# Optimization experiments

Hardware: AMD Instinct MI355X
Metric: run time of the kernel (lower is better)

Reference implementation:

```python
import jax, jax.numpy as jnp
import numpy as np

N, E, R, H = 50000, 400000, 3, 3
IN, HID, OUT, C, B = 128, 64, 64, 16, 8


def _deg_norm(idx):
    # DGL GraphConv norm='both': deg.clamp(min=1) ** -0.5
    deg = jax.ops.segment_sum(jnp.ones(idx.shape, jnp.float32), idx, N)
    return jnp.maximum(deg, 1.0) ** -0.5


def _graph_conv(h, W, b, s, d):
    # h: [N, ..., F_in]; norm by src out-degree, matmul, scatter-sum to dst, norm by dst in-degree
    ns, nd = _deg_norm(s), _deg_norm(d)
    bshape = (N,) + (1,) * (h.ndim - 1)
    hw = (h * ns.reshape(bshape)) @ W
    agg = jax.ops.segment_sum(hw[s], d, N)
    return agg * nd.reshape(bshape) + b


def _gat(h, W, al, ar, b, s, d):
    # h: [N, HID] -> [N, H, HID] multi-head GAT with edge softmax over incoming edges
    f = (h @ W).reshape(N, H, HID)
    el = jnp.sum(f * al, axis=-1)  # [N, H]
    er = jnp.sum(f * ar, axis=-1)  # [N, H]
    e = jax.nn.leaky_relu(el[s] + er[d], 0.2)  # [E, H]
    m = jax.ops.segment_max(e, d, N)
    ez = jnp.exp(e - m[d])
    z = jax.ops.segment_sum(ez, d, N)
    alpha = ez / (z[d] + 1e-9)  # [E, H]
    out = jax.ops.segment_sum(alpha[:, :, None] * f[s], d, N)  # [N, H, HID]
    return out + b.reshape(H, HID)


def setup_inputs() -> dict:
    key = jax.random.key(0)
    k = jax.random.split(key, 12)
    s = 0.05
    return {
        "x": jax.random.normal(k[0], (N, IN), jnp.float32),
        "src": jax.random.randint(k[1], (R, E), 0, N, jnp.int32),
        "dst": jax.random.randint(k[2], (R, E), 0, N, jnp.int32),
        "graph_id": (jnp.arange(N, dtype=jnp.int32) * B // N).astype(jnp.int32),
        "W1": jax.random.normal(k[3], (R, IN, HID), jnp.float32) * s,
        "b1": jnp.zeros((R, HID), jnp.float32),
        "Wg": jax.random.normal(k[4], (R, HID, H * HID), jnp.float32) * s,
        "al": jax.random.normal(k[5], (R, H, HID), jnp.float32) * s,
        "ar": jax.random.normal(k[6], (R, H, HID), jnp.float32) * s,
        "bg": jnp.zeros((R, H * HID), jnp.float32),
        "W2": jax.random.normal(k[7], (R, HID, OUT), jnp.float32) * s,
        "b2": jnp.zeros((R, OUT), jnp.float32),
        "Wc": jax.random.normal(k[8], (OUT, C), jnp.float32) * s,
        "bc": jnp.zeros((C,), jnp.float32),
    }


def reference(x, src, dst, graph_id, W1, b1, Wg, al, ar, bg, W2, b2, Wc, bc):
    # conv1: per-relation GraphConv, aggregate='sum'
    h = sum(_graph_conv(x, W1[r], b1[r], src[r], dst[r]) for r in range(R))  # [N, HID]
    # F.normalize (L2 over dim=1, eps=1e-12)
    h = h / jnp.maximum(jnp.linalg.norm(h, axis=1, keepdims=True), 1e-12)
    # gatconv: per-relation GAT (3 heads), aggregate='sum'
    h = sum(_gat(h, Wg[r], al[r], ar[r], bg[r], src[r], dst[r]) for r in range(R))  # [N, H, HID]
    h = jax.nn.relu(h)
    # dropout(0.3) omitted: deterministic eval reference
    # conv2: GraphConv applied per head
    h = sum(_graph_conv(h, W2[r], b2[r], src[r], dst[r]) for r in range(R))  # [N, H, OUT]
    h = jax.nn.sigmoid(h)
    # dgl.mean_nodes over batched graphs
    cnt = jax.ops.segment_sum(jnp.ones((N,), jnp.float32), graph_id, B)
    pooled = jax.ops.segment_sum(h, graph_id, B) / jnp.maximum(cnt, 1.0)[:, None, None]  # [B, H, OUT]
    hg = jax.nn.sigmoid(pooled @ Wc + bc)  # [B, H, C]
    return jnp.mean(hg, axis=2)  # [B, H]
```

## Files before the change

kernel.cpp:

```cpp
#include <hip/hip_runtime.h>
#include <math.h>

#define NN 50000
#define EE 400000
#define RR 3
#define NH 3
#define FIN 128
#define HID 64
#define FOUT 64
#define NC 16
#define NB 8
#define NGAT 208

typedef __attribute__((ext_vector_type(8))) short v8s;
typedef __attribute__((ext_vector_type(4))) float v4f;
typedef unsigned short u16;
typedef unsigned char u8;
typedef unsigned int u32;
typedef __attribute__((ext_vector_type(4))) unsigned short u16x4;

#define QS 32.0f
#define IQS (1.0f / 32.0f)

__device__ __forceinline__ u16 f2b(float f) {
  unsigned u = __float_as_uint(f);
  return (u16)((u + 0x7fffu + ((u >> 16) & 1u)) >> 16);
}
__device__ __forceinline__ float b2f(u16 b) {
  return __uint_as_float(((unsigned)b) << 16);
}
__device__ __forceinline__ float wexp(float e) {
  e = e > 0.f ? e : 0.2f * e;
  return __expf(e);
}
__device__ __forceinline__ u8 f2e(float v) {
  return (u8)(__builtin_amdgcn_cvt_pk_fp8_f32(v, 0.f, 0, false) & 0xff);
}

__global__ void k_deg(const int* __restrict__ src, const int* __restrict__ dst,
                      int* __restrict__ degs, int* __restrict__ degd) {
  int i = blockIdx.x * 256 + threadIdx.x;
  if (i >= RR * EE) return;
  int r = i / EE;
  atomicAdd(&degs[r * NN + src[i]], 1);
  atomicAdd(&degd[r * NN + dst[i]], 1);
}

__global__ void k_norm(const int* __restrict__ degs, const int* __restrict__ degd,
                       float* __restrict__ ns, float* __restrict__ nd) {
  int i = blockIdx.x * 256 + threadIdx.x;
  if (i >= RR * NN) return;
  ns[i] = 1.0f / sqrtf((float)(degs[i] > 1 ? degs[i] : 1));
  nd[i] = 1.0f / sqrtf((float)(degd[i] > 1 ? degd[i] : 1));
}

__global__ void k_scan1(const int* __restrict__ deg, int* __restrict__ offs,
                        int* __restrict__ bsum) {
  __shared__ int sh[256];
  int gid = blockIdx.x * 256 + threadIdx.x;
  int v = (gid < RR * NN) ? deg[gid] : 0;
  sh[threadIdx.x] = v;
  __syncthreads();
  for (int off = 1; off < 256; off <<= 1) {
    int t = (threadIdx.x >= off) ? sh[threadIdx.x - off] : 0;
    __syncthreads();
    sh[threadIdx.x] += t;
    __syncthreads();
  }
  if (gid < RR * NN) offs[gid] = sh[threadIdx.x] - v;
  if (threadIdx.x == 255) bsum[blockIdx.x] = sh[255];
}

__global__ void k_scan2(int* __restrict__ bsum, int nb) {
  __shared__ int sh[1024];
  int v = (threadIdx.x < nb) ? bsum[threadIdx.x] : 0;
  sh[threadIdx.x] = v;
  __syncthreads();
  for (int off = 1; off < 1024; off <<= 1) {
    int t = (threadIdx.x >= off) ? sh[threadIdx.x - off] : 0;
    __syncthreads();
    sh[threadIdx.x] += t;
    __syncthreads();
  }
  if (threadIdx.x < nb) bsum[threadIdx.x] = sh[threadIdx.x] - v;
}

__global__ void k_scan3(int* __restrict__ offs, const int* __restrict__ bsum,
                        int* __restrict__ cursor) {
  int i = blockIdx.x * 256 + threadIdx.x;
  if (i >= RR * NN) return;
  int v = offs[i] + bsum[i / 256];
  offs[i] = v;
  cursor[i] = v;
}

__global__ void k_fill(const int* __restrict__ src, const int* __restrict__ dst,
                       int* __restrict__ cursor, int* __restrict__ esrc,
                       int* __restrict__ edst) {
  int i = blockIdx.x * 256 + threadIdx.x;
  if (i >= RR * EE) return;
  int r = i / EE;
  int d = dst[i];
  int pos = atomicAdd(&cursor[r * NN + d], 1);
  esrc[pos] = src[i];
  edst[pos] = d;
}

__global__ void k_cast(const float4* __restrict__ in, u16x4* __restrict__ out, int n4) {
  int i = blockIdx.x * 256 + threadIdx.x;
  if (i >= n4) return;
  float4 v = in[i];
  u16x4 o;
  o.x = f2b(v.x); o.y = f2b(v.y); o.z = f2b(v.z); o.w = f2b(v.w);
  out[i] = o;
}

__global__ void k_bcomp(const float* __restrict__ Wg, const float* __restrict__ al,
                        const float* __restrict__ ar, float* __restrict__ B) {
  int i = blockIdx.x * 256 + threadIdx.x;
  if (i >= RR * HID * NGAT) return;
  int col = i % NGAT;
  int k = (i / NGAT) % HID;
  int r = i / (NGAT * HID);
  float v = 0.f;
  if (col < NH * HID) {
    v = Wg[((size_t)(r * HID + k)) * (NH * HID) + col];
  } else if (col < NH * HID + 6) {
    int c2 = col - NH * HID;
    int isar = c2 / NH, h = c2 % NH;
    const float* wg = Wg + ((size_t)(r * HID + k)) * (NH * HID) + h * HID;
    const float* av = (isar ? ar : al) + (r * NH + h) * HID;
    float a = 0.f;
#pragma unroll 8
    for (int c = 0; c < HID; ++c) a += wg[c] * av[c];
    v = a;
  }
  B[i] = v;
}

template <int K, int N, int OUTMODE>
__global__ __launch_bounds__(256) void k_gemm(const u16* __restrict__ A, int lda,
                                              const float* __restrict__ B0, int bstr,
                                              void* __restrict__ C0,
                                              u16* __restrict__ elr,
                                              const float* __restrict__ s0, int M) {
  constexpr int KP = K + 8;
  __shared__ __align__(16) u16 Bt[N * KP];
  int y = blockIdx.y;
  int rrel = (OUTMODE == 3) ? y / NH : y;
  int head = (OUTMODE == 3) ? y % NH : 0;
  const float* B = B0 + (size_t)rrel * bstr;
  const float* scale = s0 + (size_t)rrel * NN;
  const u16* Ab = A + head * HID;
  for (int i = threadIdx.x; i < K * N; i += 256) {
    int k = i / N, n = i % N;
    Bt[n * KP + k] = f2b(B[(size_t)k * N + n]);
  }
  __syncthreads();
  int wid = threadIdx.x >> 6, lane = threadIdx.x & 63;
  int l15 = lane & 15, lg = lane >> 4;
  constexpr int NT = N / 16;
  int ntiles = (M + 63) >> 6;
  for (int tile = blockIdx.x; tile < ntiles; tile += gridDim.x) {
    int mbase = tile * 64 + wid * 16;
    v4f acc[NT];
#pragma unroll
    for (int t = 0; t < NT; ++t) acc[t] = (v4f)(0.f);
    int arow = mbase + l15;
    if (arow >= M) arow = M - 1;
    const u16* ap = Ab + (size_t)arow * lda + lg * 8;
#pragma unroll
    for (int ks = 0; ks < K / 32; ++ks) {
      v8s a = *(const v8s*)(ap + ks * 32);
#pragma unroll
      for (int t = 0; t < NT; ++t) {
        v8s b = *(const v8s*)(&Bt[(t * 16 + l15) * KP + lg * 8 + ks * 32]);
        acc[t] = __builtin_amdgcn_mfma_f32_16x16x32_bf16(a, b, acc[t], 0, 0, 0);
      }
    }
#pragma unroll
    for (int q = 0; q < 4; ++q) {
      int row = mbase + lg * 4 + q;
      if (row >= M) continue;
      if (OUTMODE == 1) {
        float s = scale[row] * QS;
        u8* C = (u8*)C0 + ((size_t)y * M + row) * 64;
#pragma unroll
        for (int t = 0; t < NT; ++t) C[t * 16 + l15] = f2e(acc[t][q] * s);
      } else if (OUTMODE == 2) {
        u32* C = (u32*)C0 + ((size_t)y * M + row) * 64;
#pragma unroll
        for (int tm = 0; tm < 4; ++tm) {
          u32 pk = __builtin_amdgcn_cvt_pk_fp8_f32(acc[tm][q] * QS,
                                                   acc[tm + 4][q] * QS, 0, false);
          pk = __builtin_amdgcn_cvt_pk_fp8_f32(acc[tm + 8][q] * QS, 0.f, pk, true);
          C[tm * 16 + l15] = pk;
        }
        if (l15 < 6)
          elr[((size_t)y * M + row) * 8 + (l15 < 3 ? l15 : l15 + 1)] =
              f2b(acc[12][q]);
      } else {
        float s = scale[row] * QS;
        u8* C = (u8*)C0 + (((size_t)rrel * M + row) * 64) * 4 + head;
#pragma unroll
        for (int t = 0; t < NT; ++t) C[(t * 16 + l15) * 4] = f2e(acc[t][q] * s);
      }
    }
  }
}

__global__ void k_g1(const int* __restrict__ offs, const int* __restrict__ degd,
                     const int* __restrict__ esrc, const u8* __restrict__ c1pk,
                     const float* __restrict__ nd, const float* __restrict__ b1,
                     u16* __restrict__ h1b) {
  int node = blockIdx.x * 4 + (threadIdx.x >> 6);
  int lane = threadIdx.x & 63;
  if (node >= NN) return;
  float v = 0.f;
#pragma unroll
  for (int r = 0; r < RR; ++r) {
    int start = offs[r * NN + node];
    int deg = degd[r * NN + node];
    const u8* base = c1pk + (size_t)r * NN * 64 + lane;
    float t = 0.f;
    int j = 0;
    for (; j + 4 <= deg; j += 4) {
      int s0 = esrc[start + j], s1 = esrc[start + j + 1];
      int s2 = esrc[start + j + 2], s3 = esrc[start + j + 3];
      float a0 = __builtin_amdgcn_cvt_f32_fp8((u32)base[(size_t)s0 * 64], 0);
      float a1 = __builtin_amdgcn_cvt_f32_fp8((u32)base[(size_t)s1 * 64], 0);
      float a2 = __builtin_amdgcn_cvt_f32_fp8((u32)base[(size_t)s2 * 64], 0);
      float a3 = __builtin_amdgcn_cvt_f32_fp8((u32)base[(size_t)s3 * 64], 0);
      t += (a0 + a1) + (a2 + a3);
    }
    for (; j < deg; ++j)
      t += __builtin_amdgcn_cvt_f32_fp8((u32)base[(size_t)esrc[start + j] * 64], 0);
    v += t * nd[r * NN + node];
  }
  v = v * IQS + b1[lane] + b1[HID + lane] + b1[2 * HID + lane];
  float sq = v * v;
  for (int off = 32; off; off >>= 1) sq += __shfl_xor(sq, off);
  float nrm = sqrtf(sq);
  nrm = nrm > 1e-12f ? nrm : 1e-12f;
  h1b[node * HID + lane] = f2b(v / nrm);
}

__global__ void k_ew(const int* __restrict__ esrc, const int* __restrict__ edst,
                     const u16* __restrict__ elr, u16* __restrict__ ew) {
  int i = blockIdx.x * 256 + threadIdx.x;
  if (i >= RR * EE) return;
  int r = i / EE;
  int s = esrc[i], d = edst[i];
  const u16* es = elr + ((size_t)(r * NN + s)) * 8;
  const u16* ed = elr + ((size_t)(r * NN + d)) * 8 + 4;
  u16x4 o;
  o.x = f2b(wexp(b2f(es[0]) + b2f(ed[0])));
  o.y = f2b(wexp(b2f(es[1]) + b2f(ed[1])));
  o.z = f2b(wexp(b2f(es[2]) + b2f(ed[2])));
  o.w = 0;
  *(u16x4*)(ew + (size_t)i * 4) = o;
}

__global__ void k_gatg(const int* __restrict__ offs, const int* __restrict__ degd,
                       const int* __restrict__ esrc, const u32* __restrict__ fpk,
                       const u16* __restrict__ ew, const float* __restrict__ bg,
                       u16* __restrict__ gatb) {
  int node = blockIdx.x * 4 + (threadIdx.x >> 6);
  int lane = threadIdx.x & 63;
  if (node >= NN) return;
  float o0 = 0.f, o1 = 0.f, o2 = 0.f;
#pragma unroll
  for (int r = 0; r < RR; ++r) {
    const u32* f = fpk + (size_t)r * NN * 64 + lane;
    int start = offs[r * NN + node];
    int deg = degd[r * NN + node];
    float z0 = 0.f, z1 = 0.f, z2 = 0.f;
    float a0 = 0.f, a1 = 0.f, a2 = 0.f;
    int j = 0;
    for (; j + 4 <= deg; j += 4) {
      int p = start + j;
      int s0 = esrc[p], s1 = esrc[p + 1], s2 = esrc[p + 2], s3 = esrc[p + 3];
      u16x4 wa = *(const u16x4*)(ew + (size_t)p * 4);
      u16x4 wb = *(const u16x4*)(ew + (size_t)(p + 1) * 4);
      u16x4 wc = *(const u16x4*)(ew + (size_t)(p + 2) * 4);
      u16x4 wd = *(const u16x4*)(ew + (size_t)(p + 3) * 4);
      u32 v0 = f[(size_t)s0 * 64];
      u32 v1 = f[(size_t)s1 * 64];
      u32 v2 = f[(size_t)s2 * 64];
      u32 v3 = f[(size_t)s3 * 64];
      float w;
      w = b2f(wa.x); z0 += w; a0 += w * __builtin_amdgcn_cvt_f32_fp8(v0, 0);
      w = b2f(wa.y); z1 += w; a1 += w * __builtin_amdgcn_cvt_f32_fp8(v0, 1);
      w = b2f(wa.z); z2 += w; a2 += w * __builtin_amdgcn_cvt_f32_fp8(v0, 2);
      w = b2f(wb.x); z0 += w; a0 += w * __builtin_amdgcn_cvt_f32_fp8(v1, 0);
      w = b2f(wb.y); z1 += w; a1 += w * __builtin_amdgcn_cvt_f32_fp8(v1, 1);
      w = b2f(wb.z); z2 += w; a2 += w * __builtin_amdgcn_cvt_f32_fp8(v1, 2);
      w = b2f(wc.x); z0 += w; a0 += w * __builtin_amdgcn_cvt_f32_fp8(v2, 0);
      w = b2f(wc.y); z1 += w; a1 += w * __builtin_amdgcn_cvt_f32_fp8(v2, 1);
      w = b2f(wc.z); z2 += w; a2 += w * __builtin_amdgcn_cvt_f32_fp8(v2, 2);
      w = b2f(wd.x); z0 += w; a0 += w * __builtin_amdgcn_cvt_f32_fp8(v3, 0);
      w = b2f(wd.y); z1 += w; a1 += w * __builtin_amdgcn_cvt_f32_fp8(v3, 1);
      w = b2f(wd.z); z2 += w; a2 += w * __builtin_amdgcn_cvt_f32_fp8(v3, 2);
    }
    for (; j < deg; ++j) {
      int p = start + j;
      u16x4 wa = *(const u16x4*)(ew + (size_t)p * 4);
      u32 v0 = f[(size_t)esrc[p] * 64];
      float w;
      w = b2f(wa.x); z0 += w; a0 += w * __builtin_amdgcn_cvt_f32_fp8(v0, 0);
      w = b2f(wa.y); z1 += w; a1 += w * __builtin_amdgcn_cvt_f32_fp8(v0, 1);
      w = b2f(wa.z); z2 += w; a2 += w * __builtin_amdgcn_cvt_f32_fp8(v0, 2);
    }
    o0 += a0 / (z0 + 1e-9f);
    o1 += a1 / (z1 + 1e-9f);
    o2 += a2 / (z2 + 1e-9f);
  }
  float ov[NH] = {o0, o1, o2};
#pragma unroll
  for (int h = 0; h < NH; ++h) {
    int j = h * HID + lane;
    float v = ov[h] * IQS + bg[j] + bg[NH * HID + j] + bg[2 * NH * HID + j];
    gatb[(size_t)node * (NH * HID) + j] = f2b(fmaxf(v, 0.f));
  }
}

__global__ void k_g2(const int* __restrict__ offs, const int* __restrict__ degd,
                     const int* __restrict__ esrc, const u32* __restrict__ c2pk,
                     const float* __restrict__ nd, const float* __restrict__ b2,
                     u16* __restrict__ agg2b) {
  int node = blockIdx.x * 4 + (threadIdx.x >> 6);
  int lane = threadIdx.x & 63;
  if (node >= NN) return;
  float o0 = 0.f, o1 = 0.f, o2 = 0.f;
#pragma unroll
  for (int r = 0; r < RR; ++r) {
    const u32* hw = c2pk + (size_t)r * NN * 64 + lane;
    int start = offs[r * NN + node];
    int deg = degd[r * NN + node];
    float a0 = 0.f, a1 = 0.f, a2 = 0.f;
    int j = 0;
    for (; j + 4 <= deg; j += 4) {
      int p = start + j;
      u32 v0 = hw[(size_t)esrc[p] * 64];
      u32 v1 = hw[(size_t)esrc[p + 1] * 64];
      u32 v2 = hw[(size_t)esrc[p + 2] * 64];
      u32 v3 = hw[(size_t)esrc[p + 3] * 64];
      a0 += (__builtin_amdgcn_cvt_f32_fp8(v0, 0) + __builtin_amdgcn_cvt_f32_fp8(v1, 0)) +
            (__builtin_amdgcn_cvt_f32_fp8(v2, 0) + __builtin_amdgcn_cvt_f32_fp8(v3, 0));
      a1 += (__builtin_amdgcn_cvt_f32_fp8(v0, 1) + __builtin_amdgcn_cvt_f32_fp8(v1, 1)) +
            (__builtin_amdgcn_cvt_f32_fp8(v2, 1) + __builtin_amdgcn_cvt_f32_fp8(v3, 1));
      a2 += (__builtin_amdgcn_cvt_f32_fp8(v0, 2) + __builtin_amdgcn_cvt_f32_fp8(v1, 2)) +
            (__builtin_amdgcn_cvt_f32_fp8(v2, 2) + __builtin_amdgcn_cvt_f32_fp8(v3, 2));
    }
    for (; j < deg; ++j) {
      u32 v0 = hw[(size_t)esrc[start + j] * 64];
      a0 += __builtin_amdgcn_cvt_f32_fp8(v0, 0);
      a1 += __builtin_amdgcn_cvt_f32_fp8(v0, 1);
      a2 += __builtin_amdgcn_cvt_f32_fp8(v0, 2);
    }
    float ndv = nd[r * NN + node];
    o0 += a0 * ndv; o1 += a1 * ndv; o2 += a2 * ndv;
  }
  float b2s = b2[lane] + b2[FOUT + lane] + b2[2 * FOUT + lane];
  float ov[NH] = {o0, o1, o2};
#pragma unroll
  for (int h = 0; h < NH; ++h) {
    float v = 1.0f / (1.0f + __expf(-(ov[h] * IQS + b2s)));
    agg2b[(size_t)node * (NH * FOUT) + h * FOUT + lane] = f2b(v);
  }
}

__global__ void k_cnt2(const int* __restrict__ gid, float* __restrict__ cnt) {
  __shared__ int loc[NB];
  if (threadIdx.x < NB) loc[threadIdx.x] = 0;
  __syncthreads();
  int i = blockIdx.x * 256 + threadIdx.x;
  if (i < NN) atomicAdd(&loc[gid[i]], 1);
  __syncthreads();
  if (threadIdx.x < NB) atomicAdd(&cnt[threadIdx.x], (float)loc[threadIdx.x]);
}

__global__ void k_pool(const u16* __restrict__ h3, const int* __restrict__ gid,
                       float* __restrict__ pooled) {
  int j = threadIdx.x;
  int start = blockIdx.x * 128;
  if (start >= NN) return;
  int end = start + 128;
  if (end > NN) end = NN;
  int gcur = gid[start];
  float acc = 0.f;
  for (int n = start; n < end; ++n) {
    int g = gid[n];
    if (g != gcur) {
      atomicAdd(&pooled[gcur * (NH * FOUT) + j], acc);
      acc = 0.f;
      gcur = g;
    }
    acc += b2f(h3[(size_t)n * (NH * FOUT) + j]);
  }
  atomicAdd(&pooled[gcur * (NH * FOUT) + j], acc);
}

__global__ void k_final(const float* __restrict__ pooled, const float* __restrict__ cnt,
                        const float* __restrict__ Wc, const float* __restrict__ bc,
                        float* __restrict__ out) {
  int t = threadIdx.x;
  if (t >= NB * NH) return;
  int b = t / NH;
  float inv = 1.0f / fmaxf(cnt[b], 1.0f);
  const float* p = pooled + t * FOUT;
  float sacc = 0.f;
  for (int c = 0; c < NC; ++c) {
    float acc = bc[c];
    for (int o = 0; o < FOUT; ++o) acc += p[o] * inv * Wc[o * NC + c];
    sacc += 1.0f / (1.0f + __expf(-acc));
  }
  out[t] = sacc * (1.0f / NC);
}

extern "C" void kernel_launch(void* const* d_in, const int* in_sizes, int n_in,
                              void* d_out, int out_size, void* d_ws, size_t ws_size,
                              hipStream_t stream) {
  const float* x = (const float*)d_in[0];
  const int* src = (const int*)d_in[1];
  const int* dst = (const int*)d_in[2];
  const int* gid = (const int*)d_in[3];
  const float* W1 = (const float*)d_in[4];
  const float* b1 = (const float*)d_in[5];
  const float* Wg = (const float*)d_in[6];
  const float* al = (const float*)d_in[7];
  const float* ar = (const float*)d_in[8];
  const float* bg = (const float*)d_in[9];
  const float* W2 = (const float*)d_in[10];
  const float* b2 = (const float*)d_in[11];
  const float* Wc = (const float*)d_in[12];
  const float* bc = (const float*)d_in[13];
  float* out = (float*)d_out;

  int* degs = (int*)d_ws;
  int* degd = degs + RR * NN;
  float* cnt = (float*)(degd + RR * NN);
  float* pooled = cnt + NB;
  size_t zero_bytes = ((size_t)2 * RR * NN + NB + NB * NH * FOUT) * 4;
  int* offs = (int*)(pooled + NB * NH * FOUT);
  int* cursor = offs + RR * NN + 8;
  int* bsum = cursor + RR * NN;
  int* esrc = bsum + 1024;
  int* edst = esrc + (size_t)RR * EE;
  float* ns = (float*)(edst + (size_t)RR * EE);
  float* nd = ns + RR * NN;
  float* Bcomp = nd + RR * NN;
  u16* elr = (u16*)(Bcomp + RR * HID * NGAT);
  u16* ew = elr + (size_t)RR * NN * 8;
  u16* xb = ew + (size_t)RR * EE * 4;
  u16* h1b = xb + (size_t)NN * FIN;
  u8* c1pk = (u8*)(h1b + (size_t)NN * HID);
  u16* gatb = (u16*)(c1pk + (size_t)RR * NN * 64);
  u32* fpk = (u32*)(gatb + (size_t)NN * NH * HID);
  u32* c2pk = fpk;
  u16* agg2b = xb;

  hipMemsetAsync(d_ws, 0, zero_bytes, stream);

  const int nscan = RR * NN;
  const int nblk1 = (nscan + 255) / 256;

  k_deg<<<(RR * EE + 255) / 256, 256, 0, stream>>>(src, dst, degs, degd);
  k_norm<<<(nscan + 255) / 256, 256, 0, stream>>>(degs, degd, ns, nd);
  k_scan1<<<nblk1, 256, 0, stream>>>(degd, offs, bsum);
  k_scan2<<<1, 1024, 0, stream>>>(bsum, nblk1);
  k_scan3<<<nblk1, 256, 0, stream>>>(offs, bsum, cursor);
  k_fill<<<(RR * EE + 255) / 256, 256, 0, stream>>>(src, dst, cursor, esrc, edst);

  k_cast<<<(NN * FIN / 4 + 255) / 256, 256, 0, stream>>>((const float4*)x, (u16x4*)xb,
                                                         NN * FIN / 4);
  k_bcomp<<<(RR * HID * NGAT + 255) / 256, 256, 0, stream>>>(Wg, al, ar, Bcomp);

  k_gemm<FIN, HID, 1><<<dim3(782, RR), 256, 0, stream>>>(
      xb, FIN, W1, FIN * HID, c1pk, nullptr, ns, NN);
  k_g1<<<(NN + 3) / 4, 256, 0, stream>>>(offs, degd, esrc, c1pk, nd, b1, h1b);

  k_gemm<HID, NGAT, 2><<<dim3(782, RR), 256, 0, stream>>>(
      h1b, HID, Bcomp, HID * NGAT, fpk, elr, ns, NN);
  k_ew<<<(RR * EE + 255) / 256, 256, 0, stream>>>(esrc, edst, elr, ew);
  k_gatg<<<(NN + 3) / 4, 256, 0, stream>>>(offs, degd, esrc, fpk, ew, bg, gatb);

  k_gemm<HID, FOUT, 3><<<dim3(782, RR * NH), 256, 0, stream>>>(
      gatb, NH * HID, W2, HID * FOUT, c2pk, nullptr, ns, NN);
  k_g2<<<(NN + 3) / 4, 256, 0, stream>>>(offs, degd, esrc, c2pk, nd, b2, agg2b);

  k_cnt2<<<(NN + 255) / 256, 256, 0, stream>>>(gid, cnt);
  k_pool<<<(NN + 127) / 128, 192, 0, stream>>>(agg2b, gid, pooled);
  k_final<<<1, 64, 0, stream>>>(pooled, cnt, Wc, bc, out);
}
```

Measured before the change: 666.9 us.

## Build CSR with LDS-privatized histograms and deterministic placement instead of global atomics

Replaces the global-atomic degree count and atomic cursor fill with per-chunk shared-memory histograms over node ranges, a reduction that produces per-block prefix offsets, and a placement kernel that writes edges by offset+block prefix+rank. This removes contended global atomics and the edst array. The edge-weight kernel now iterates per destination node over CSR rows, which makes it node-parallel with variable-length loops. The change adds extra passes and large u16 partial arrays (aliased over fpk) that cost memory traffic.

```diff
diff --git a/kernel.cpp b/kernel.cpp
--- a/kernel.cpp
+++ b/kernel.cpp
@@ -12,6 +12,11 @@
 #define NB 8
 #define NGAT 208
 
+#define NBLK 32
+#define CHK (EE / NBLK)
+#define NRNG 4
+#define RNGSZ (NN / NRNG)
+
 typedef __attribute__((ext_vector_type(8))) short v8s;
 typedef __attribute__((ext_vector_type(4))) float v4f;
 typedef unsigned short u16;
@@ -37,21 +42,51 @@
   return (u8)(__builtin_amdgcn_cvt_pk_fp8_f32(v, 0.f, 0, false) & 0xff);
 }
 
-__global__ void k_deg(const int* __restrict__ src, const int* __restrict__ dst,
-                      int* __restrict__ degs, int* __restrict__ degd) {
-  int i = blockIdx.x * 256 + threadIdx.x;
-  if (i >= RR * EE) return;
-  int r = i / EE;
-  atomicAdd(&degs[r * NN + src[i]], 1);
-  atomicAdd(&degd[r * NN + dst[i]], 1);
-}
-
-__global__ void k_norm(const int* __restrict__ degs, const int* __restrict__ degd,
-                       float* __restrict__ ns, float* __restrict__ nd) {
+__global__ __launch_bounds__(1024) void k_hist(const int* __restrict__ src,
+                                               const int* __restrict__ dst,
+                                               u16* __restrict__ ps,
+                                               u16* __restrict__ pd,
+                                               u16* __restrict__ rank) {
+  __shared__ u32 h[RNGSZ];
+  int b = blockIdx.x;
+  int kind = blockIdx.y >> 2, range = blockIdx.y & 3;
+  int r = blockIdx.z;
+  int lo = range * RNGSZ;
+  for (int i = threadIdx.x; i < RNGSZ; i += 1024) h[i] = 0;
+  __syncthreads();
+  int base = r * EE + b * CHK;
+  if (kind) {
+    for (int i = threadIdx.x; i < CHK; i += 1024) {
+      int d = dst[base + i] - lo;
+      if ((unsigned)d < RNGSZ) rank[base + i] = (u16)atomicAdd(&h[d], 1u);
+    }
+  } else {
+    for (int i = threadIdx.x; i < CHK; i += 1024) {
+      int s = src[base + i] - lo;
+      if ((unsigned)s < RNGSZ) atomicAdd(&h[s], 1u);
+    }
+  }
+  __syncthreads();
+  u16* p = (kind ? pd : ps) + (size_t)(r * NBLK + b) * NN + lo;
+  for (int i = threadIdx.x; i < RNGSZ; i += 1024) p[i] = (u16)h[i];
+}
+
+__global__ void k_red(const u16* __restrict__ ps, const u16* __restrict__ pd,
+                      int* __restrict__ degd, float* __restrict__ ns,
+                      float* __restrict__ nd, u16* __restrict__ bpfx) {
   int i = blockIdx.x * 256 + threadIdx.x;
   if (i >= RR * NN) return;
-  ns[i] = 1.0f / sqrtf((float)(degs[i] > 1 ? degs[i] : 1));
-  nd[i] = 1.0f / sqrtf((float)(degd[i] > 1 ? degd[i] : 1));
+  int r = i / NN, n = i - r * NN;
+  u32 ss = 0, sd = 0;
+  for (int b = 0; b < NBLK; ++b) {
+    size_t o = (size_t)(r * NBLK + b) * NN + n;
+    ss += ps[o];
+    bpfx[o] = (u16)sd;
+    sd += pd[o];
+  }
+  degd[i] = (int)sd;
+  ns[i] = 1.0f / sqrtf((float)(ss > 1 ? ss : 1));
+  nd[i] = 1.0f / sqrtf((float)(sd > 1 ? sd : 1));
 }
 
 __global__ void k_scan1(const int* __restrict__ deg, int* __restrict__ offs,
@@ -85,25 +120,32 @@
   if (threadIdx.x < nb) bsum[threadIdx.x] = sh[threadIdx.x] - v;
 }
 
-__global__ void k_scan3(int* __restrict__ offs, const int* __restrict__ bsum,
-                        int* __restrict__ cursor) {
+__global__ void k_scan3(int* __restrict__ offs, const int* __restrict__ bsum) {
   int i = blockIdx.x * 256 + threadIdx.x;
   if (i >= RR * NN) return;
-  int v = offs[i] + bsum[i / 256];
-  offs[i] = v;
-  cursor[i] = v;
-}
-
-__global__ void k_fill(const int* __restrict__ src, const int* __restrict__ dst,
-                       int* __restrict__ cursor, int* __restrict__ esrc,
-                       int* __restrict__ edst) {
-  int i = blockIdx.x * 256 + threadIdx.x;
-  if (i >= RR * EE) return;
-  int r = i / EE;
-  int d = dst[i];
-  int pos = atomicAdd(&cursor[r * NN + d], 1);
-  esrc[pos] = src[i];
-  edst[pos] = d;
+  offs[i] = offs[i] + bsum[i / 256];
+}
+
+__global__ __launch_bounds__(1024) void k_place(const int* __restrict__ src,
+                                                const int* __restrict__ dst,
+                                                const int* __restrict__ offs,
+                                                const u16* __restrict__ bpfx,
+                                                const u16* __restrict__ rank,
+                                                int* __restrict__ esrc) {
+  int b = blockIdx.x;
+  int range = blockIdx.y;
+  int r = blockIdx.z;
+  int lo = range * RNGSZ;
+  int base = r * EE + b * CHK;
+  for (int i = threadIdx.x; i < CHK; i += 1024) {
+    int d = dst[base + i] - lo;
+    if ((unsigned)d < RNGSZ) {
+      int dg = d + lo;
+      size_t o = (size_t)(r * NBLK + b) * NN + dg;
+      int pos = offs[r * NN + dg] + (int)bpfx[o] + (int)rank[base + i];
+      esrc[pos] = src[base + i];
+    }
+  }
 }
 
 __global__ void k_cast(const float4* __restrict__ in, u16x4* __restrict__ out, int n4) {
@@ -245,20 +287,25 @@
   h1b[node * HID + lane] = f2b(v / nrm);
 }
 
-__global__ void k_ew(const int* __restrict__ esrc, const int* __restrict__ edst,
-                     const u16* __restrict__ elr, u16* __restrict__ ew) {
+__global__ void k_ew(const int* __restrict__ offs, const int* __restrict__ degd,
+                     const int* __restrict__ esrc, const u16* __restrict__ elr,
+                     u16* __restrict__ ew) {
   int i = blockIdx.x * 256 + threadIdx.x;
-  if (i >= RR * EE) return;
-  int r = i / EE;
-  int s = esrc[i], d = edst[i];
-  const u16* es = elr + ((size_t)(r * NN + s)) * 8;
-  const u16* ed = elr + ((size_t)(r * NN + d)) * 8 + 4;
-  u16x4 o;
-  o.x = f2b(wexp(b2f(es[0]) + b2f(ed[0])));
-  o.y = f2b(wexp(b2f(es[1]) + b2f(ed[1])));
-  o.z = f2b(wexp(b2f(es[2]) + b2f(ed[2])));
-  o.w = 0;
-  *(u16x4*)(ew + (size_t)i * 4) = o;
+  if (i >= RR * NN) return;
+  int r = i / NN;
+  int start = offs[i], deg = degd[i];
+  const u16* ed = elr + (size_t)i * 8 + 4;
+  float e0 = b2f(ed[0]), e1 = b2f(ed[1]), e2 = b2f(ed[2]);
+  for (int j = 0; j < deg; ++j) {
+    int s = esrc[start + j];
+    const u16* es = elr + ((size_t)r * NN + s) * 8;
+    u16x4 o;
+    o.x = f2b(wexp(b2f(es[0]) + e0));
+    o.y = f2b(wexp(b2f(es[1]) + e1));
+    o.z = f2b(wexp(b2f(es[2]) + e2));
+    o.w = 0;
+    *(u16x4*)(ew + (size_t)(start + j) * 4) = o;
+  }
 }
 
 __global__ void k_gatg(const int* __restrict__ offs, const int* __restrict__ degd,
@@ -437,17 +484,14 @@
   const float* bc = (const float*)d_in[13];
   float* out = (float*)d_out;
 
-  int* degs = (int*)d_ws;
-  int* degd = degs + RR * NN;
-  float* cnt = (float*)(degd + RR * NN);
+  float* cnt = (float*)d_ws;
   float* pooled = cnt + NB;
-  size_t zero_bytes = ((size_t)2 * RR * NN + NB + NB * NH * FOUT) * 4;
-  int* offs = (int*)(pooled + NB * NH * FOUT);
-  int* cursor = offs + RR * NN + 8;
-  int* bsum = cursor + RR * NN;
+  size_t zero_bytes = ((size_t)NB + NB * NH * FOUT) * 4;
+  int* degd = (int*)(pooled + NB * NH * FOUT);
+  int* offs = degd + RR * NN;
+  int* bsum = offs + RR * NN + 8;
   int* esrc = bsum + 1024;
-  int* edst = esrc + (size_t)RR * EE;
-  float* ns = (float*)(edst + (size_t)RR * EE);
+  float* ns = (float*)(esrc + (size_t)RR * EE);
   float* nd = ns + RR * NN;
   float* Bcomp = nd + RR * NN;
   u16* elr = (u16*)(Bcomp + RR * HID * NGAT);
@@ -459,18 +503,22 @@
   u32* fpk = (u32*)(gatb + (size_t)NN * NH * HID);
   u32* c2pk = fpk;
   u16* agg2b = xb;
+  u16* ps = (u16*)fpk;
+  u16* pd = ps + (size_t)RR * NBLK * NN;
+  u16* bpfx = pd + (size_t)RR * NBLK * NN;
+  u16* rank = bpfx + (size_t)RR * NBLK * NN;
 
   hipMemsetAsync(d_ws, 0, zero_bytes, stream);
 
   const int nscan = RR * NN;
   const int nblk1 = (nscan + 255) / 256;
 
-  k_deg<<<(RR * EE + 255) / 256, 256, 0, stream>>>(src, dst, degs, degd);
-  k_norm<<<(nscan + 255) / 256, 256, 0, stream>>>(degs, degd, ns, nd);
+  k_hist<<<dim3(NBLK, 8, RR), 1024, 0, stream>>>(src, dst, ps, pd, rank);
+  k_red<<<nblk1, 256, 0, stream>>>(ps, pd, degd, ns, nd, bpfx);
   k_scan1<<<nblk1, 256, 0, stream>>>(degd, offs, bsum);
   k_scan2<<<1, 1024, 0, stream>>>(bsum, nblk1);
-  k_scan3<<<nblk1, 256, 0, stream>>>(offs, bsum, cursor);
-  k_fill<<<(RR * EE + 255) / 256, 256, 0, stream>>>(src, dst, cursor, esrc, edst);
+  k_scan3<<<nblk1, 256, 0, stream>>>(offs, bsum);
+  k_place<<<dim3(NBLK, NRNG, RR), 1024, 0, stream>>>(src, dst, offs, bpfx, rank, esrc);
 
   k_cast<<<(NN * FIN / 4 + 255) / 256, 256, 0, stream>>>((const float4*)x, (u16x4*)xb,
                                                          NN * FIN / 4);
@@ -482,7 +530,7 @@
 
   k_gemm<HID, NGAT, 2><<<dim3(782, RR), 256, 0, stream>>>(
       h1b, HID, Bcomp, HID * NGAT, fpk, elr, ns, NN);
-  k_ew<<<(RR * EE + 255) / 256, 256, 0, stream>>>(esrc, edst, elr, ew);
+  k_ew<<<nblk1, 256, 0, stream>>>(offs, degd, esrc, elr, ew);
   k_gatg<<<(NN + 3) / 4, 256, 0, stream>>>(offs, degd, esrc, fpk, ew, bg, gatb);
 
   k_gemm<HID, FOUT, 3><<<dim3(782, RR * NH), 256, 0, stream>>>(
```

New measurement: 552.8 us. 1.21x faster.
